# Optimization experiments

Hardware: AMD Instinct MI355X
Metric: run time of the kernel (lower is better)

Reference implementation:

```python
import jax, jax.numpy as jnp
import numpy as np

R, N, F, H, C = 3, 100000, 256, 128, 2
N0, S1, D1, S2, D2 = 16384, 16384, 4096, 4096, 512


def setup_inputs() -> dict:
    key = jax.random.key(0)
    ks = jax.random.split(key, 13)
    return {
        "features": jax.random.normal(ks[0], (N, F), jnp.float32),
        "src_nodes": jax.random.randint(ks[1], (R, N0), 0, N),
        "dstsrc2src1": jax.random.randint(ks[2], (R, S1), 0, N0),
        "dstsrc2dst1": jax.random.randint(ks[3], (R, D1), 0, N0),
        "dif_mat1": jax.random.uniform(ks[4], (R, D1, S1), jnp.float32) / S1,
        "dstsrc2src2": jax.random.randint(ks[5], (R, S2), 0, D1),
        "dstsrc2dst2": jax.random.randint(ks[6], (R, D2), 0, D1),
        "dif_mat2": jax.random.uniform(ks[7], (R, D2, S2), jnp.float32) / S2,
        "w1": jax.random.normal(ks[8], (2 * F, H), jnp.float32) * 0.05,
        "w2": jax.random.normal(ks[9], (2 * H, H), jnp.float32) * 0.05,
        "relation_vectors": jax.random.uniform(ks[10], (R, H), jnp.float32),
        "attention_vec": jax.random.uniform(ks[11], (2 * H, 1), jnp.float32),
        "classifier_w": jax.random.normal(ks[12], (H, C), jnp.float32) * 0.05,
    }


def _agg(x, d2s, d2d, dif, w, rel_vec, att_vec):
    # x: [n, din]; dif: [d, s]; w: [2*din, H]
    agg = dif @ x[d2s]                                  # mean-diffused neighbor feats [d, din]
    h = jnp.concatenate([agg, x[d2d]], axis=1) @ w      # [d, H]
    rel = jnp.broadcast_to(rel_vec[None, :], (h.shape[0], rel_vec.shape[0]))
    score = (jnp.concatenate([h, rel], axis=1) @ att_vec)[:, 0]  # [d]
    att = jax.nn.softmax(score)                         # softmax over batch nodes
    return h * att[:, None]


def reference(features, src_nodes, dstsrc2src1, dstsrc2dst1, dif_mat1,
              dstsrc2src2, dstsrc2dst2, dif_mat2, w1, w2,
              relation_vectors, attention_vec, classifier_w):
    def per_relation(src, s1, d1, m1, s2, d2, m2, rel_vec):
        x = features[src]                               # gather node feats [N0, F]
        x = _agg(x, s1, d1, m1, w1, rel_vec, attention_vec)   # [D1, H]
        x = _agg(x, s2, d2, m2, w2, rel_vec, attention_vec)   # [D2, H]
        return x

    xs = jax.vmap(per_relation)(src_nodes, dstsrc2src1, dstsrc2dst1, dif_mat1,
                                dstsrc2src2, dstsrc2dst2, dif_mat2, relation_vectors)
    summed = jnp.sum(xs, axis=0)                        # sum over relations [D2, H]
    inv_norm = jax.lax.rsqrt(jnp.maximum(jnp.sum(summed * summed, axis=1, keepdims=True), 1e-12))
    normed = summed * inv_norm                          # tf.nn.l2_normalize(axis=1)
    return jax.nn.softmax(normed @ classifier_w, axis=-1)
```

## Files before the change

### kernel.cpp

```cpp
#include <hip/hip_runtime.h>
#include <hip/hip_bf16.h>
#include <math.h>

constexpr int Rc  = 3;
constexpr int Fc  = 256;
constexpr int Hc  = 128;
constexpr int N0c = 16384;
constexpr int S1c = 16384;
constexpr int D1c = 4096;
constexpr int S2c = 4096;
constexpr int D2c = 512;
constexpr int KH1 = 4;
constexpr int KH2 = 16;

typedef __bf16 bf16x8 __attribute__((ext_vector_type(8)));
typedef float  f32x4  __attribute__((ext_vector_type(4)));

__device__ __forceinline__ void glds16(const void* g, void* l) {
  __builtin_amdgcn_global_load_lds(
      (const __attribute__((address_space(1))) void*)g,
      (__attribute__((address_space(3))) void*)l, 16, 0, 0);
}

__device__ __forceinline__ bf16x8 cvt2(const float4 a, const float4 b) {
  bf16x8 c;
  c[0] = (__bf16)a.x; c[1] = (__bf16)a.y; c[2] = (__bf16)a.z; c[3] = (__bf16)a.w;
  c[4] = (__bf16)b.x; c[5] = (__bf16)b.y; c[6] = (__bf16)b.z; c[7] = (__bf16)b.w;
  return c;
}

__device__ __forceinline__ unsigned short bfbits(float v) {
  __bf16 b = (__bf16)v; unsigned short u;
  __builtin_memcpy(&u, &b, 2); return u;
}

__global__ __launch_bounds__(256, 2)
void wpack(const float* __restrict__ w1, const float* __restrict__ w2,
           unsigned char* __restrict__ wp) {
  const int tile = blockIdx.x, half = blockIdx.y, t = threadIdx.x;
  const float* src; int row0;
  if (tile < 4)       { src = w1; row0 = tile * 64; }
  else if (tile < 8)  { src = w1; row0 = 256 + (tile - 4) * 64; }
  else if (tile < 10) { src = w2; row0 = (tile - 8) * 64; }
  else                { src = w2; row0 = 128 + (tile - 10) * 64; }
  unsigned char* dst = wp + ((size_t)half * 12 + tile) * 16384;
  __shared__ float sm[64][132];
  {
    const int r = t >> 2, c0 = (t & 3) * 32;
#pragma unroll
    for (int j = 0; j < 8; j++)
      *(float4*)&sm[r][c0 + 4 * j] = *(const float4*)(src + (size_t)(row0 + r) * 128 + c0 + 4 * j);
  }
  __syncthreads();
  if (t < 128) {
    const int n = t;
#pragma unroll
    for (int ch = 0; ch < 8; ch++) {
      bf16x8 o;
#pragma unroll
      for (int e = 0; e < 8; e++) {
        float v = sm[ch * 8 + e][n];
        __bf16 h = (__bf16)v;
        o[e] = half ? (__bf16)(v - (float)h) : h;
      }
      *(bf16x8*)(dst + n * 128 + ((ch ^ (n & 7)) * 16)) = o;
    }
  }
}

__global__ __launch_bounds__(256, 3)
void gg_layer1(const float* __restrict__ feat, const int* __restrict__ srcn,
               const int* __restrict__ d2s1, const int* __restrict__ d2d1,
               const unsigned char* __restrict__ wp,
               unsigned char* __restrict__ xgwp, float* __restrict__ xdw) {
  const int rel = blockIdx.y;
  int bx = blockIdx.x;
  const int job = bx >= 256 ? 1 : 0;
  if (job) bx -= 256;
  const int s0 = bx * 64;
  const int rows = job ? D1c : S1c;
  const int* idx = job ? d2d1 : d2s1;
  const unsigned char* Bh = wp + (size_t)(job ? 4 : 0) * 16384;
  const unsigned char* Bl = wp + (size_t)(12 + (job ? 4 : 0)) * 16384;

  const int t = threadIdx.x, lane = t & 63, w = t >> 6;
  const int NT = 4;
  const int mh = w >> 1, nh = w & 1;

  __shared__ __bf16 Asm[64 * 64];
  __shared__ __bf16 Bhs[128 * 64];
  __shared__ __bf16 Bls[128 * 64];

  const int arow = t >> 2, ak0 = (t & 3) * 16;
  const int row = s0 + arow;
  const size_t arowg = (size_t)srcn[rel * N0c + idx[(size_t)rel * rows + row]];
  const float* aptr = feat + arowg * Fc + ak0;
  const int ac0 = ak0 >> 3;
  __bf16* asw0 = &Asm[arow * 64 + ((ac0    ) ^ (arow & 7)) * 8];
  __bf16* asw1 = &Asm[arow * 64 + ((ac0 + 1) ^ (arow & 7)) * 8];

  f32x4 acc[2][4] = {};

  for (int tl = 0; tl < NT; ++tl) {
    asm volatile("s_waitcnt lgkmcnt(0)" ::: "memory");
    __builtin_amdgcn_s_barrier();
    __builtin_amdgcn_sched_barrier(0);
    {
      const unsigned char* bh = Bh + (size_t)tl * 16384 + w * 4096 + lane * 16;
      const unsigned char* bl = Bl + (size_t)tl * 16384 + w * 4096 + lane * 16;
      char* dh = (char*)Bhs + w * 4096;
      char* dl = (char*)Bls + w * 4096;
#pragma unroll
      for (int i = 0; i < 4; i++) glds16(bh + i * 1024, dh + i * 1024);
#pragma unroll
      for (int i = 0; i < 4; i++) glds16(bl + i * 1024, dl + i * 1024);
    }
    {
      float4 a[4];
#pragma unroll
      for (int j = 0; j < 4; j++) a[j] = *(const float4*)(aptr + tl * 64 + 4 * j);
      *(bf16x8*)asw0 = cvt2(a[0], a[1]);
      *(bf16x8*)asw1 = cvt2(a[2], a[3]);
    }
    asm volatile("s_waitcnt vmcnt(0) lgkmcnt(0)" ::: "memory");
    __builtin_amdgcn_s_barrier();
    __builtin_amdgcn_sched_barrier(0);
#pragma unroll
    for (int ks = 0; ks < 2; ks++) {
      const int ch = ks * 4 + (lane >> 4);
      bf16x8 af[2], bh[4], bl[4];
#pragma unroll
      for (int mi = 0; mi < 2; mi++) {
        int r = mh * 32 + mi * 16 + (lane & 15);
        af[mi] = *(const bf16x8*)&Asm[r * 64 + ((ch ^ (r & 7)) * 8)];
      }
#pragma unroll
      for (int ni = 0; ni < 4; ni++) {
        int n = nh * 64 + ni * 16 + (lane & 15);
        bh[ni] = *(const bf16x8*)&Bhs[n * 64 + ((ch ^ (n & 7)) * 8)];
        bl[ni] = *(const bf16x8*)&Bls[n * 64 + ((ch ^ (n & 7)) * 8)];
      }
#pragma unroll
      for (int mi = 0; mi < 2; mi++)
#pragma unroll
        for (int ni = 0; ni < 4; ni++) {
          acc[mi][ni] = __builtin_amdgcn_mfma_f32_16x16x32_bf16(af[mi], bh[ni], acc[mi][ni], 0, 0, 0);
          acc[mi][ni] = __builtin_amdgcn_mfma_f32_16x16x32_bf16(af[mi], bl[ni], acc[mi][ni], 0, 0, 0);
        }
    }
  }
  if (job) {
#pragma unroll
    for (int mi = 0; mi < 2; mi++)
#pragma unroll
      for (int ni = 0; ni < 4; ni++) {
        const int col = nh * 64 + ni * 16 + (lane & 15);
#pragma unroll
        for (int j = 0; j < 4; j++) {
          const int r = mh * 32 + mi * 16 + (lane >> 4) * 4 + j;
          xdw[((size_t)rel * D1c + s0 + r) * 128 + col] = acc[mi][ni][j];
        }
      }
  } else {
    unsigned char* tile = xgwp + ((size_t)(rel * (S1c >> 6) + bx)) * 16384;
#pragma unroll
    for (int mi = 0; mi < 2; mi++)
#pragma unroll
      for (int ni = 0; ni < 4; ni++) {
        const int sl0 = mh * 32 + mi * 16 + (lane >> 4) * 4;
        const int n = nh * 64 + ni * 16 + (lane & 15);
        const int ch = sl0 >> 3, e0 = sl0 & 7, cs = ch ^ (n & 7);
        ushort4 u;
        u.x = bfbits(acc[mi][ni][0]); u.y = bfbits(acc[mi][ni][1]);
        u.z = bfbits(acc[mi][ni][2]); u.w = bfbits(acc[mi][ni][3]);
        *(ushort4*)(tile + n * 128 + cs * 16 + e0 * 2) = u;
      }
  }
}

__global__ __launch_bounds__(256, 3)
void gg_layer2(const float* __restrict__ h1, const float* __restrict__ scl,
               const unsigned char* __restrict__ wp,
               float* __restrict__ P, float* __restrict__ Q) {
  const int rel = blockIdx.y, s0 = blockIdx.x * 64, z = blockIdx.z;
  const unsigned char* Bh = wp + (size_t)(z ? 10 : 8) * 16384;
  const unsigned char* Bl = wp + (size_t)(z ? 22 : 20) * 16384;
  float* Cf = z ? Q : P;

  const int t = threadIdx.x, lane = t & 63, w = t >> 6;
  const int NT = 2;
  const int mh = w >> 1, nh = w & 1;

  __shared__ __bf16 Asm[64 * 64];
  __shared__ __bf16 Bhs[128 * 64];
  __shared__ __bf16 Bls[128 * 64];

  const int arow = t >> 2, ak0 = (t & 3) * 16;
  const int row = s0 + arow;
  const float* aptr = h1 + ((size_t)rel * D1c + row) * Hc + ak0;
  const float sc = scl[(size_t)rel * D1c + row];
  const int ac0 = ak0 >> 3;
  __bf16* asw0 = &Asm[arow * 64 + ((ac0    ) ^ (arow & 7)) * 8];
  __bf16* asw1 = &Asm[arow * 64 + ((ac0 + 1) ^ (arow & 7)) * 8];

  f32x4 acc[2][4] = {};

  for (int tl = 0; tl < NT; ++tl) {
    asm volatile("s_waitcnt lgkmcnt(0)" ::: "memory");
    __builtin_amdgcn_s_barrier();
    __builtin_amdgcn_sched_barrier(0);
    {
      const unsigned char* bh = Bh + (size_t)tl * 16384 + w * 4096 + lane * 16;
      const unsigned char* bl = Bl + (size_t)tl * 16384 + w * 4096 + lane * 16;
      char* dh = (char*)Bhs + w * 4096;
      char* dl = (char*)Bls + w * 4096;
#pragma unroll
      for (int i = 0; i < 4; i++) glds16(bh + i * 1024, dh + i * 1024);
#pragma unroll
      for (int i = 0; i < 4; i++) glds16(bl + i * 1024, dl + i * 1024);
    }
    {
      float4 a[4];
#pragma unroll
      for (int j = 0; j < 4; j++) a[j] = *(const float4*)(aptr + tl * 64 + 4 * j);
#pragma unroll
      for (int j = 0; j < 4; j++) { a[j].x *= sc; a[j].y *= sc; a[j].z *= sc; a[j].w *= sc; }
      *(bf16x8*)asw0 = cvt2(a[0], a[1]);
      *(bf16x8*)asw1 = cvt2(a[2], a[3]);
    }
    asm volatile("s_waitcnt vmcnt(0) lgkmcnt(0)" ::: "memory");
    __builtin_amdgcn_s_barrier();
    __builtin_amdgcn_sched_barrier(0);
#pragma unroll
    for (int ks = 0; ks < 2; ks++) {
      const int ch = ks * 4 + (lane >> 4);
      bf16x8 af[2], bh[4], bl[4];
#pragma unroll
      for (int mi = 0; mi < 2; mi++) {
        int r = mh * 32 + mi * 16 + (lane & 15);
        af[mi] = *(const bf16x8*)&Asm[r * 64 + ((ch ^ (r & 7)) * 8)];
      }
#pragma unroll
      for (int ni = 0; ni < 4; ni++) {
        int n = nh * 64 + ni * 16 + (lane & 15);
        bh[ni] = *(const bf16x8*)&Bhs[n * 64 + ((ch ^ (n & 7)) * 8)];
        bl[ni] = *(const bf16x8*)&Bls[n * 64 + ((ch ^ (n & 7)) * 8)];
      }
#pragma unroll
      for (int mi = 0; mi < 2; mi++)
#pragma unroll
        for (int ni = 0; ni < 4; ni++) {
          acc[mi][ni] = __builtin_amdgcn_mfma_f32_16x16x32_bf16(af[mi], bh[ni], acc[mi][ni], 0, 0, 0);
          acc[mi][ni] = __builtin_amdgcn_mfma_f32_16x16x32_bf16(af[mi], bl[ni], acc[mi][ni], 0, 0, 0);
        }
    }
  }
#pragma unroll
  for (int mi = 0; mi < 2; mi++)
#pragma unroll
    for (int ni = 0; ni < 4; ni++) {
      const int col = nh * 64 + ni * 16 + (lane & 15);
#pragma unroll
      for (int j = 0; j < 4; j++) {
        const int r = mh * 32 + mi * 16 + (lane >> 4) * 4 + j;
        Cf[((size_t)rel * D1c + s0 + r) * 128 + col] = acc[mi][ni][j];
      }
    }
}

template <int SWZ>
__global__ __launch_bounds__(256, 3)
void gemm_big(const float* __restrict__ A, const unsigned char* __restrict__ Bp,
              float* __restrict__ C, int M, int KTOT, int KH) {
  int rel, kh, m0;
  if (SWZ) {
    const int F = blockIdx.x;
    const int xcd = F & 7, r = F >> 3;
    const int sub = r >> 5, m = r & 31;
    const int h = xcd + 8 * sub;
    const int g = h >> 1;
    rel = g >> 2; kh = g & 3;
    m0 = ((h & 1) * 32 + m) * 64;
  } else {
    rel = blockIdx.z; kh = blockIdx.y; m0 = blockIdx.x * 64;
  }
  const int t = threadIdx.x, lane = t & 63, w = t >> 6;
  const int KB = KTOT / KH, NT = KB >> 6;
  const int mh = w >> 1, nh = w & 1;

  const float* Ag = A + ((size_t)rel * M + m0) * KTOT + (size_t)kh * KB;
  const unsigned char* Bt = Bp + ((size_t)rel * (KTOT >> 6) + (size_t)kh * NT) * 16384;
  float* Cg = C + (((size_t)kh * Rc + rel) * M + m0) * 128;

  __shared__ __bf16 Asm[64 * 64];
  __shared__ __bf16 Bsm[2][128 * 64];

  f32x4 acc[2][4] = {};
  const int arow = t >> 2, ak0 = (t & 3) * 16;
  const float* aptr = Ag + (size_t)arow * KTOT + ak0;
  const int ac0 = ak0 >> 3;
  __bf16* asw0 = &Asm[arow * 64 + ((ac0    ) ^ (arow & 7)) * 8];
  __bf16* asw1 = &Asm[arow * 64 + ((ac0 + 1) ^ (arow & 7)) * 8];
  const unsigned char* bsrc = Bt + w * 4096 + lane * 16;

  float4 a0[4], a1[4];
#pragma unroll
  for (int j = 0; j < 4; j++) a0[j] = *(const float4*)(aptr + 4 * j);
  {
    char* bd = (char*)Bsm[0] + w * 4096;
#pragma unroll
    for (int i = 0; i < 4; i++) glds16(bsrc + i * 1024, bd + i * 1024);
  }

  for (int tl = 0; tl < NT; ++tl) {
    const int cur = tl & 1;
    asm volatile("s_waitcnt lgkmcnt(0)" ::: "memory");
    __builtin_amdgcn_s_barrier();
    __builtin_amdgcn_sched_barrier(0);
    if (tl + 1 < NT) {
      const unsigned char* bs = bsrc + (size_t)(tl + 1) * 16384;
      char* bd = (char*)Bsm[cur ^ 1] + w * 4096;
#pragma unroll
      for (int i = 0; i < 4; i++) glds16(bs + i * 1024, bd + i * 1024);
      const float* ap = aptr + (size_t)(tl + 1) * 64;
#pragma unroll
      for (int j = 0; j < 4; j++) a1[j] = *(const float4*)(ap + 4 * j);
    }
    *(bf16x8*)asw0 = cvt2(a0[0], a0[1]);
    *(bf16x8*)asw1 = cvt2(a0[2], a0[3]);
    if (tl + 1 < NT)
      asm volatile("s_waitcnt vmcnt(8) lgkmcnt(0)" ::: "memory");
    else
      asm volatile("s_waitcnt vmcnt(0) lgkmcnt(0)" ::: "memory");
    __builtin_amdgcn_s_barrier();
    __builtin_amdgcn_sched_barrier(0);
    const __bf16* Bc = Bsm[cur];
#pragma unroll
    for (int ks = 0; ks < 2; ks++) {
      const int ch = ks * 4 + (lane >> 4);
      bf16x8 af[2], bfr[4];
#pragma unroll
      for (int mi = 0; mi < 2; mi++) {
        int r = mh * 32 + mi * 16 + (lane & 15);
        af[mi] = *(const bf16x8*)&Asm[r * 64 + ((ch ^ (r & 7)) * 8)];
      }
#pragma unroll
      for (int ni = 0; ni < 4; ni++) {
        int n = nh * 64 + ni * 16 + (lane & 15);
        bfr[ni] = *(const bf16x8*)&Bc[n * 64 + ((ch ^ (n & 7)) * 8)];
      }
#pragma unroll
      for (int mi = 0; mi < 2; mi++)
#pragma unroll
        for (int ni = 0; ni < 4; ni++)
          acc[mi][ni] = __builtin_amdgcn_mfma_f32_16x16x32_bf16(af[mi], bfr[ni], acc[mi][ni], 0, 0, 0);
    }
#pragma unroll
    for (int j = 0; j < 4; j++) a0[j] = a1[j];
  }
#pragma unroll
  for (int mi = 0; mi < 2; mi++)
#pragma unroll
    for (int ni = 0; ni < 4; ni++) {
      const int col = nh * 64 + ni * 16 + (lane & 15);
#pragma unroll
      for (int j = 0; j < 4; j++) {
        const int r = mh * 32 + mi * 16 + (lane >> 4) * 4 + j;
        Cg[(size_t)r * 128 + col] = acc[mi][ni][j];
      }
    }
}

__global__ __launch_bounds__(256, 2)
void pgpack(const float* __restrict__ P, const int* __restrict__ d2s2,
            unsigned char* __restrict__ PGp) {
  const int rel = blockIdx.y, kb = blockIdx.x, t = threadIdx.x;
  __shared__ __bf16 sm[64][136];
  {
    const int kl = t >> 2, c0 = (t & 3) * 32;
    const int sr = d2s2[rel * S2c + kb * 64 + kl];
    const float4* p = (const float4*)(P + ((size_t)rel * D1c + sr) * 128 + c0);
#pragma unroll
    for (int j = 0; j < 4; j++)
      *(bf16x8*)&sm[kl][c0 + 8 * j] = cvt2(p[2 * j], p[2 * j + 1]);
  }
  __syncthreads();
  if (t < 128) {
    const int n = t;
    unsigned char* dst = PGp + ((size_t)(rel * (S2c >> 6) + kb)) * 16384;
#pragma unroll
    for (int ch = 0; ch < 8; ch++) {
      bf16x8 o;
#pragma unroll
      for (int e = 0; e < 8; e++) o[e] = sm[ch * 8 + e][n];
      *(bf16x8*)(dst + n * 128 + ((ch ^ (n & 7)) * 16)) = o;
    }
  }
}

__global__ __launch_bounds__(128, 4)
void combine1(const float* __restrict__ aggP, const float* __restrict__ xdw,
              const float* __restrict__ attv, float* __restrict__ h1,
              float* __restrict__ score1) {
  const int rel = blockIdx.y, d0 = blockIdx.x * 8, t = threadIdx.x;
  float acc[8];
#pragma unroll
  for (int i = 0; i < 8; i++) {
    const int d = d0 + i;
    float v = xdw[((size_t)rel * D1c + d) * 128 + t];
#pragma unroll
    for (int p = 0; p < KH1; p++)
      v += aggP[(((size_t)p * Rc + rel) * D1c + d) * 128 + t];
    acc[i] = v;
    h1[((size_t)rel * D1c + d) * 128 + t] = v;
  }
  const float avt = attv[t];
  __shared__ float sred[2][8];
#pragma unroll
  for (int i = 0; i < 8; i++) {
    float p = acc[i] * avt;
    p += __shfl_down(p, 32); p += __shfl_down(p, 16); p += __shfl_down(p, 8);
    p += __shfl_down(p, 4);  p += __shfl_down(p, 2);  p += __shfl_down(p, 1);
    if ((t & 63) == 0) sred[t >> 6][i] = p;
  }
  __syncthreads();
  if (t < 8) score1[rel * D1c + d0 + t] = sred[0][t] + sred[1][t];
}

__global__ __launch_bounds__(128, 4)
void combine2(const float* __restrict__ aggP2, const float* __restrict__ Q,
              const int* __restrict__ d2d2, const float* __restrict__ attv,
              float* __restrict__ h2, float* __restrict__ score2) {
  const int rel = blockIdx.y, d0 = blockIdx.x * 8, t = threadIdx.x;
  float acc[8];
#pragma unroll
  for (int i = 0; i < 8; i++) {
    const int d = d0 + i;
    const int qr = d2d2[rel * D2c + d];
    float v = Q[((size_t)rel * D1c + qr) * 128 + t];
#pragma unroll
    for (int p = 0; p < KH2; p++)
      v += aggP2[(((size_t)p * Rc + rel) * D2c + d) * 128 + t];
    acc[i] = v;
    h2[((size_t)rel * D2c + d) * 128 + t] = v;
  }
  const float avt = attv[t];
  __shared__ float sred[2][8];
#pragma unroll
  for (int i = 0; i < 8; i++) {
    float p = acc[i] * avt;
    p += __shfl_down(p, 32); p += __shfl_down(p, 16); p += __shfl_down(p, 8);
    p += __shfl_down(p, 4);  p += __shfl_down(p, 2);  p += __shfl_down(p, 1);
    if ((t & 63) == 0) sred[t >> 6][i] = p;
  }
  __syncthreads();
  if (t < 8) score2[rel * D2c + d0 + t] = sred[0][t] + sred[1][t];
}

__global__ __launch_bounds__(1024, 1)
void k4_softmax1(float* __restrict__ score1) {
  const int rel = blockIdx.x, t = threadIdx.x;
  float* s = score1 + rel * D1c;
  float v[4], m = -INFINITY;
#pragma unroll
  for (int j = 0; j < 4; j++) { v[j] = s[t + j * 1024]; m = fmaxf(m, v[j]); }
  __shared__ float red[1024];
  red[t] = m; __syncthreads();
  for (int off = 512; off > 0; off >>= 1) {
    if (t < off) red[t] = fmaxf(red[t], red[t + off]);
    __syncthreads();
  }
  const float M = red[0];
  __syncthreads();
  float e[4], sum = 0.f;
#pragma unroll
  for (int j = 0; j < 4; j++) { e[j] = expf(v[j] - M); sum += e[j]; }
  red[t] = sum; __syncthreads();
  for (int off = 512; off > 0; off >>= 1) {
    if (t < off) red[t] += red[t + off];
    __syncthreads();
  }
  const float inv = 1.0f / red[0];
#pragma unroll
  for (int j = 0; j < 4; j++) s[t + j * 1024] = e[j] * inv;
}

__global__ __launch_bounds__(512, 1)
void k8_softmax2(float* __restrict__ score2) {
  const int rel = blockIdx.x, t = threadIdx.x;
  float* s = score2 + rel * D2c;
  const float v = s[t];
  __shared__ float red[512];
  red[t] = v; __syncthreads();
  for (int off = 256; off > 0; off >>= 1) {
    if (t < off) red[t] = fmaxf(red[t], red[t + off]);
    __syncthreads();
  }
  const float M = red[0];
  __syncthreads();
  const float e = expf(v - M);
  red[t] = e; __syncthreads();
  for (int off = 256; off > 0; off >>= 1) {
    if (t < off) red[t] += red[t + off];
    __syncthreads();
  }
  s[t] = e / red[0];
}

__global__ __launch_bounds__(128, 4)
void k9_final(const float* __restrict__ h2, const float* __restrict__ att2,
              const float* __restrict__ cw, float* __restrict__ out) {
  const int d = blockIdx.x, t = threadIdx.x;
  float v = 0.f;
#pragma unroll
  for (int r = 0; r < Rc; r++)
    v += h2[((size_t)r * D2c + d) * Hc + t] * att2[r * D2c + d];
  float ss = v * v;
  ss += __shfl_down(ss, 32); ss += __shfl_down(ss, 16); ss += __shfl_down(ss, 8);
  ss += __shfl_down(ss, 4);  ss += __shfl_down(ss, 2);  ss += __shfl_down(ss, 1);
  __shared__ float sr[3][2];
  if ((t & 63) == 0) sr[0][t >> 6] = ss;
  __syncthreads();
  const float tot = sr[0][0] + sr[0][1];
  const float inv = rsqrtf(fmaxf(tot, 1e-12f));
  const float nv = v * inv;
  float p0 = nv * cw[t * 2], p1 = nv * cw[t * 2 + 1];
  p0 += __shfl_down(p0, 32); p0 += __shfl_down(p0, 16); p0 += __shfl_down(p0, 8);
  p0 += __shfl_down(p0, 4);  p0 += __shfl_down(p0, 2);  p0 += __shfl_down(p0, 1);
  p1 += __shfl_down(p1, 32); p1 += __shfl_down(p1, 16); p1 += __shfl_down(p1, 8);
  p1 += __shfl_down(p1, 4);  p1 += __shfl_down(p1, 2);  p1 += __shfl_down(p1, 1);
  if ((t & 63) == 0) { sr[1][t >> 6] = p0; sr[2][t >> 6] = p1; }
  __syncthreads();
  if (t == 0) {
    const float l0 = sr[1][0] + sr[1][1];
    const float l1 = sr[2][0] + sr[2][1];
    const float m = fmaxf(l0, l1);
    const float e0 = expf(l0 - m), e1 = expf(l1 - m);
    const float is = 1.0f / (e0 + e1);
    out[d * 2 + 0] = e0 * is;
    out[d * 2 + 1] = e1 * is;
  }
}

extern "C" void kernel_launch(void* const* d_in, const int* in_sizes, int n_in,
                              void* d_out, int out_size, void* d_ws, size_t ws_size,
                              hipStream_t stream) {
  (void)in_sizes; (void)n_in; (void)out_size; (void)ws_size;
  const float* feat = (const float*)d_in[0];
  const int*   srcn = (const int*)d_in[1];
  const int*   d2s1 = (const int*)d_in[2];
  const int*   d2d1 = (const int*)d_in[3];
  const float* dif1 = (const float*)d_in[4];
  const int*   d2s2 = (const int*)d_in[5];
  const int*   d2d2 = (const int*)d_in[6];
  const float* dif2 = (const float*)d_in[7];
  const float* w1   = (const float*)d_in[8];
  const float* w2   = (const float*)d_in[9];
  const float* attv = (const float*)d_in[11];
  const float* cw   = (const float*)d_in[12];
  float* out = (float*)d_out;

  char* p = (char*)d_ws;
  auto take = [&](size_t n) { char* r = p; p += (n + 255) & ~(size_t)255; return r; };
  unsigned char* wp   = (unsigned char*)take(24 * 16384);
  unsigned char* xgwp = (unsigned char*)take((size_t)Rc * 256 * 16384);
  float* xdw    = (float*)take((size_t)Rc * D1c * 128 * 4);
  float* aggP   = (float*)take((size_t)KH1 * Rc * D1c * 128 * 4);
  float* h1     = (float*)take((size_t)Rc * D1c * 128 * 4);
  float* score1 = (float*)take((size_t)Rc * D1c * 4);
  unsigned char* PGp = (unsigned char*)take((size_t)Rc * 64 * 16384);
  float* h2     = (float*)take((size_t)Rc * D2c * 128 * 4);
  float* score2 = (float*)take((size_t)Rc * D2c * 4);
  float* P = (float*)xgwp;
  float* Q = P + (size_t)Rc * D1c * 128;
  float* aggP2 = aggP;

  wpack<<<dim3(12, 2), 256, 0, stream>>>(w1, w2, wp);
  gg_layer1<<<dim3(320, Rc), 256, 0, stream>>>(feat, srcn, d2s1, d2d1, wp, xgwp, xdw);
  gemm_big<1><<<768, 256, 0, stream>>>(dif1, xgwp, aggP, D1c, S1c, KH1);
  combine1<<<dim3(D1c / 8, Rc), 128, 0, stream>>>(aggP, xdw, attv, h1, score1);
  k4_softmax1<<<Rc, 1024, 0, stream>>>(score1);
  gg_layer2<<<dim3(D1c / 64, Rc, 2), 256, 0, stream>>>(h1, score1, wp, P, Q);
  pgpack<<<dim3(S2c / 64, Rc), 256, 0, stream>>>(P, d2s2, PGp);
  gemm_big<0><<<dim3(D2c / 64, KH2, Rc), 256, 0, stream>>>(dif2, PGp, aggP2, D2c, S2c, KH2);
  combine2<<<dim3(D2c / 8, Rc), 128, 0, stream>>>(aggP2, Q, d2d2, attv, h2, score2);
  k8_softmax2<<<Rc, 512, 0, stream>>>(score2);
  k9_final<<<D2c, 128, 0, stream>>>(h2, score2, cw, out);
}
```

Baseline: 285.0 us.

## Fuse layer-1 combine into layer-2 GEMM and defer softmax normalization

Merges combine1 and gg_layer2 into one kernel. It sums the K-split partials with xdw, computes the attention score and exp, and runs both layer-2 GEMMs directly from shared memory. The two softmax kernels go away: exp scores are accumulated by atomicAdd into per-relation sums, and the 1/sum scale is applied later in pgpack, combine2 and k9_final, since the scale commutes with the linear layer. This cuts several launches and the h1 write/read round trip, and gg_layer1 now issues all of its A loads up front. The cost is that max subtraction is skipped, so exp could overflow for large scores, and the floating-point atomics make the sums non-deterministic.

```diff
diff --git a/kernel.cpp b/kernel.cpp
--- a/kernel.cpp
+++ b/kernel.cpp
@@ -36,8 +36,9 @@
 
 __global__ __launch_bounds__(256, 2)
 void wpack(const float* __restrict__ w1, const float* __restrict__ w2,
-           unsigned char* __restrict__ wp) {
+           unsigned char* __restrict__ wp, float* __restrict__ esum) {
   const int tile = blockIdx.x, half = blockIdx.y, t = threadIdx.x;
+  if (tile == 0 && half == 0 && t < 8) esum[t] = 0.f;
   const float* src; int row0;
   if (tile < 4)       { src = w1; row0 = tile * 64; }
   else if (tile < 8)  { src = w1; row0 = 256 + (tile - 4) * 64; }
@@ -84,7 +85,6 @@
   const unsigned char* Bl = wp + (size_t)(12 + (job ? 4 : 0)) * 16384;
 
   const int t = threadIdx.x, lane = t & 63, w = t >> 6;
-  const int NT = 4;
   const int mh = w >> 1, nh = w & 1;
 
   __shared__ __bf16 Asm[64 * 64];
@@ -99,9 +99,15 @@
   __bf16* asw0 = &Asm[arow * 64 + ((ac0    ) ^ (arow & 7)) * 8];
   __bf16* asw1 = &Asm[arow * 64 + ((ac0 + 1) ^ (arow & 7)) * 8];
 
+  float4 a[16];
+#pragma unroll
+  for (int tl = 0; tl < 4; tl++)
+#pragma unroll
+    for (int j = 0; j < 4; j++) a[tl * 4 + j] = *(const float4*)(aptr + tl * 64 + 4 * j);
+
   f32x4 acc[2][4] = {};
 
-  for (int tl = 0; tl < NT; ++tl) {
+  for (int tl = 0; tl < 4; ++tl) {
     asm volatile("s_waitcnt lgkmcnt(0)" ::: "memory");
     __builtin_amdgcn_s_barrier();
     __builtin_amdgcn_sched_barrier(0);
@@ -115,13 +121,8 @@
 #pragma unroll
       for (int i = 0; i < 4; i++) glds16(bl + i * 1024, dl + i * 1024);
     }
-    {
-      float4 a[4];
-#pragma unroll
-      for (int j = 0; j < 4; j++) a[j] = *(const float4*)(aptr + tl * 64 + 4 * j);
-      *(bf16x8*)asw0 = cvt2(a[0], a[1]);
-      *(bf16x8*)asw1 = cvt2(a[2], a[3]);
-    }
+    *(bf16x8*)asw0 = cvt2(a[tl * 4 + 0], a[tl * 4 + 1]);
+    *(bf16x8*)asw1 = cvt2(a[tl * 4 + 2], a[tl * 4 + 3]);
     asm volatile("s_waitcnt vmcnt(0) lgkmcnt(0)" ::: "memory");
     __builtin_amdgcn_s_barrier();
     __builtin_amdgcn_sched_barrier(0);
@@ -176,96 +177,6 @@
         *(ushort4*)(tile + n * 128 + cs * 16 + e0 * 2) = u;
       }
   }
-}
-
-__global__ __launch_bounds__(256, 3)
-void gg_layer2(const float* __restrict__ h1, const float* __restrict__ scl,
-               const unsigned char* __restrict__ wp,
-               float* __restrict__ P, float* __restrict__ Q) {
-  const int rel = blockIdx.y, s0 = blockIdx.x * 64, z = blockIdx.z;
-  const unsigned char* Bh = wp + (size_t)(z ? 10 : 8) * 16384;
-  const unsigned char* Bl = wp + (size_t)(z ? 22 : 20) * 16384;
-  float* Cf = z ? Q : P;
-
-  const int t = threadIdx.x, lane = t & 63, w = t >> 6;
-  const int NT = 2;
-  const int mh = w >> 1, nh = w & 1;
-
-  __shared__ __bf16 Asm[64 * 64];
-  __shared__ __bf16 Bhs[128 * 64];
-  __shared__ __bf16 Bls[128 * 64];
-
-  const int arow = t >> 2, ak0 = (t & 3) * 16;
-  const int row = s0 + arow;
-  const float* aptr = h1 + ((size_t)rel * D1c + row) * Hc + ak0;
-  const float sc = scl[(size_t)rel * D1c + row];
-  const int ac0 = ak0 >> 3;
-  __bf16* asw0 = &Asm[arow * 64 + ((ac0    ) ^ (arow & 7)) * 8];
-  __bf16* asw1 = &Asm[arow * 64 + ((ac0 + 1) ^ (arow & 7)) * 8];
-
-  f32x4 acc[2][4] = {};
-
-  for (int tl = 0; tl < NT; ++tl) {
-    asm volatile("s_waitcnt lgkmcnt(0)" ::: "memory");
-    __builtin_amdgcn_s_barrier();
-    __builtin_amdgcn_sched_barrier(0);
-    {
-      const unsigned char* bh = Bh + (size_t)tl * 16384 + w * 4096 + lane * 16;
-      const unsigned char* bl = Bl + (size_t)tl * 16384 + w * 4096 + lane * 16;
-      char* dh = (char*)Bhs + w * 4096;
-      char* dl = (char*)Bls + w * 4096;
-#pragma unroll
-      for (int i = 0; i < 4; i++) glds16(bh + i * 1024, dh + i * 1024);
-#pragma unroll
-      for (int i = 0; i < 4; i++) glds16(bl + i * 1024, dl + i * 1024);
-    }
-    {
-      float4 a[4];
-#pragma unroll
-      for (int j = 0; j < 4; j++) a[j] = *(const float4*)(aptr + tl * 64 + 4 * j);
-#pragma unroll
-      for (int j = 0; j < 4; j++) { a[j].x *= sc; a[j].y *= sc; a[j].z *= sc; a[j].w *= sc; }
-      *(bf16x8*)asw0 = cvt2(a[0], a[1]);
-      *(bf16x8*)asw1 = cvt2(a[2], a[3]);
-    }
-    asm volatile("s_waitcnt vmcnt(0) lgkmcnt(0)" ::: "memory");
-    __builtin_amdgcn_s_barrier();
-    __builtin_amdgcn_sched_barrier(0);
-#pragma unroll
-    for (int ks = 0; ks < 2; ks++) {
-      const int ch = ks * 4 + (lane >> 4);
-      bf16x8 af[2], bh[4], bl[4];
-#pragma unroll
-      for (int mi = 0; mi < 2; mi++) {
-        int r = mh * 32 + mi * 16 + (lane & 15);
-        af[mi] = *(const bf16x8*)&Asm[r * 64 + ((ch ^ (r & 7)) * 8)];
-      }
-#pragma unroll
-      for (int ni = 0; ni < 4; ni++) {
-        int n = nh * 64 + ni * 16 + (lane & 15);
-        bh[ni] = *(const bf16x8*)&Bhs[n * 64 + ((ch ^ (n & 7)) * 8)];
-        bl[ni] = *(const bf16x8*)&Bls[n * 64 + ((ch ^ (n & 7)) * 8)];
-      }
-#pragma unroll
-      for (int mi = 0; mi < 2; mi++)
-#pragma unroll
-        for (int ni = 0; ni < 4; ni++) {
-          acc[mi][ni] = __builtin_amdgcn_mfma_f32_16x16x32_bf16(af[mi], bh[ni], acc[mi][ni], 0, 0, 0);
-          acc[mi][ni] = __builtin_amdgcn_mfma_f32_16x16x32_bf16(af[mi], bl[ni], acc[mi][ni], 0, 0, 0);
-        }
-    }
-  }
-#pragma unroll
-  for (int mi = 0; mi < 2; mi++)
-#pragma unroll
-    for (int ni = 0; ni < 4; ni++) {
-      const int col = nh * 64 + ni * 16 + (lane & 15);
-#pragma unroll
-      for (int j = 0; j < 4; j++) {
-        const int r = mh * 32 + mi * 16 + (lane >> 4) * 4 + j;
-        Cf[((size_t)rel * D1c + s0 + r) * 128 + col] = acc[mi][ni][j];
-      }
-    }
 }
 
 template <int SWZ>
@@ -371,18 +282,140 @@
     }
 }
 
+__global__ __launch_bounds__(256, 3)
+void c1_l2(const float* __restrict__ aggP, const float* __restrict__ xdw,
+           const float* __restrict__ attv, const unsigned char* __restrict__ wp,
+           float* __restrict__ escore1, float* __restrict__ esum,
+           float* __restrict__ P, float* __restrict__ Q) {
+  const int rel = blockIdx.y, d0 = blockIdx.x * 64;
+  const int t = threadIdx.x, lane = t & 63, w = t >> 6;
+  const int mh = w >> 1, nh = w & 1;
+
+  __shared__ __bf16 Asm[64 * 128];
+  __shared__ __bf16 Bhs[128 * 64];
+  __shared__ __bf16 Bls[128 * 64];
+  __shared__ float  sred[64];
+
+  const int r = t >> 2, c0 = (t & 3) * 32;
+  float4 x0[8];
+  {
+    const size_t base = ((size_t)rel * D1c + d0 + r) * 128 + c0;
+#pragma unroll
+    for (int j = 0; j < 8; j++) x0[j] = *(const float4*)(xdw + base + 4 * j);
+#pragma unroll
+    for (int p2 = 0; p2 < KH1; p2++) {
+      const float* ap = aggP + (((size_t)p2 * Rc + rel) * D1c + d0 + r) * 128 + c0;
+#pragma unroll
+      for (int j = 0; j < 8; j++) {
+        float4 u = *(const float4*)(ap + 4 * j);
+        x0[j].x += u.x; x0[j].y += u.y; x0[j].z += u.z; x0[j].w += u.w;
+      }
+    }
+  }
+  float sp = 0.f;
+#pragma unroll
+  for (int j = 0; j < 8; j++) {
+    sp += x0[j].x * attv[c0 + 4 * j]     + x0[j].y * attv[c0 + 4 * j + 1]
+        + x0[j].z * attv[c0 + 4 * j + 2] + x0[j].w * attv[c0 + 4 * j + 3];
+  }
+  sp += __shfl_xor(sp, 1); sp += __shfl_xor(sp, 2);
+  const float e = expf(sp);
+  if ((t & 3) == 0) { escore1[(size_t)rel * D1c + d0 + r] = e; sred[r] = e; }
+  const int ch0 = (t & 3) * 4;
+#pragma unroll
+  for (int q = 0; q < 4; q++) {
+    *(bf16x8*)&Asm[r * 128 + (((ch0 + q) ^ (r & 7)) * 8)] = cvt2(x0[2 * q], x0[2 * q + 1]);
+  }
+  __syncthreads();
+  if (t < 64) {
+    float v = sred[t];
+    v += __shfl_down(v, 32); v += __shfl_down(v, 16); v += __shfl_down(v, 8);
+    v += __shfl_down(v, 4);  v += __shfl_down(v, 2);  v += __shfl_down(v, 1);
+    if (t == 0) atomicAdd(esum + rel, v);
+  }
+  f32x4 accP[2][4] = {}, accQ[2][4] = {};
+#pragma unroll
+  for (int z = 0; z < 2; z++) {
+#pragma unroll
+    for (int tl = 0; tl < 2; tl++) {
+      if (!(z == 0 && tl == 0)) {
+        asm volatile("s_waitcnt lgkmcnt(0)" ::: "memory");
+        __builtin_amdgcn_s_barrier();
+        __builtin_amdgcn_sched_barrier(0);
+      }
+      {
+        const unsigned char* bh = wp + (size_t)(8 + z * 2 + tl) * 16384 + w * 4096 + lane * 16;
+        const unsigned char* bl = wp + (size_t)(20 + z * 2 + tl) * 16384 + w * 4096 + lane * 16;
+        char* dh = (char*)Bhs + w * 4096;
+        char* dl = (char*)Bls + w * 4096;
+#pragma unroll
+        for (int i = 0; i < 4; i++) glds16(bh + i * 1024, dh + i * 1024);
+#pragma unroll
+        for (int i = 0; i < 4; i++) glds16(bl + i * 1024, dl + i * 1024);
+      }
+      asm volatile("s_waitcnt vmcnt(0) lgkmcnt(0)" ::: "memory");
+      __builtin_amdgcn_s_barrier();
+      __builtin_amdgcn_sched_barrier(0);
+      f32x4 (*acc)[4] = z ? accQ : accP;
+#pragma unroll
+      for (int ks = 0; ks < 2; ks++) {
+        const int lch = ks * 4 + (lane >> 4);
+        const int ch  = tl * 8 + lch;
+        bf16x8 af[2], bh[4], bl[4];
+#pragma unroll
+        for (int mi = 0; mi < 2; mi++) {
+          int rr = mh * 32 + mi * 16 + (lane & 15);
+          af[mi] = *(const bf16x8*)&Asm[rr * 128 + ((ch ^ (rr & 7)) * 8)];
+        }
+#pragma unroll
+        for (int ni = 0; ni < 4; ni++) {
+          int n = nh * 64 + ni * 16 + (lane & 15);
+          bh[ni] = *(const bf16x8*)&Bhs[n * 64 + ((lch ^ (n & 7)) * 8)];
+          bl[ni] = *(const bf16x8*)&Bls[n * 64 + ((lch ^ (n & 7)) * 8)];
+        }
+#pragma unroll
+        for (int mi = 0; mi < 2; mi++)
+#pragma unroll
+          for (int ni = 0; ni < 4; ni++) {
+            acc[mi][ni] = __builtin_amdgcn_mfma_f32_16x16x32_bf16(af[mi], bh[ni], acc[mi][ni], 0, 0, 0);
+            acc[mi][ni] = __builtin_amdgcn_mfma_f32_16x16x32_bf16(af[mi], bl[ni], acc[mi][ni], 0, 0, 0);
+          }
+      }
+    }
+  }
+#pragma unroll
+  for (int mi = 0; mi < 2; mi++)
+#pragma unroll
+    for (int ni = 0; ni < 4; ni++) {
+      const int col = nh * 64 + ni * 16 + (lane & 15);
+#pragma unroll
+      for (int j = 0; j < 4; j++) {
+        const int rr = mh * 32 + mi * 16 + (lane >> 4) * 4 + j;
+        P[((size_t)rel * D1c + d0 + rr) * 128 + col] = accP[mi][ni][j];
+        Q[((size_t)rel * D1c + d0 + rr) * 128 + col] = accQ[mi][ni][j];
+      }
+    }
+}
+
 __global__ __launch_bounds__(256, 2)
 void pgpack(const float* __restrict__ P, const int* __restrict__ d2s2,
+            const float* __restrict__ escore1, const float* __restrict__ esum,
             unsigned char* __restrict__ PGp) {
   const int rel = blockIdx.y, kb = blockIdx.x, t = threadIdx.x;
+  const float inv1 = 1.0f / esum[rel];
   __shared__ __bf16 sm[64][136];
   {
     const int kl = t >> 2, c0 = (t & 3) * 32;
     const int sr = d2s2[rel * S2c + kb * 64 + kl];
+    const float sc = escore1[(size_t)rel * D1c + sr] * inv1;
     const float4* p = (const float4*)(P + ((size_t)rel * D1c + sr) * 128 + c0);
 #pragma unroll
-    for (int j = 0; j < 4; j++)
-      *(bf16x8*)&sm[kl][c0 + 8 * j] = cvt2(p[2 * j], p[2 * j + 1]);
+    for (int j = 0; j < 4; j++) {
+      float4 v0 = p[2 * j], v1 = p[2 * j + 1];
+      v0.x *= sc; v0.y *= sc; v0.z *= sc; v0.w *= sc;
+      v1.x *= sc; v1.y *= sc; v1.z *= sc; v1.w *= sc;
+      *(bf16x8*)&sm[kl][c0 + 8 * j] = cvt2(v0, v1);
+    }
   }
   __syncthreads();
   if (t < 128) {
@@ -399,20 +432,24 @@
 }
 
 __global__ __launch_bounds__(128, 4)
-void combine1(const float* __restrict__ aggP, const float* __restrict__ xdw,
-              const float* __restrict__ attv, float* __restrict__ h1,
-              float* __restrict__ score1) {
+void combine2(const float* __restrict__ aggP2, const float* __restrict__ Q,
+              const int* __restrict__ d2d2, const float* __restrict__ attv,
+              const float* __restrict__ escore1, const float* __restrict__ esum,
+              float* __restrict__ h2, float* __restrict__ escore2) {
   const int rel = blockIdx.y, d0 = blockIdx.x * 8, t = threadIdx.x;
+  const float inv1 = 1.0f / esum[rel];
   float acc[8];
 #pragma unroll
   for (int i = 0; i < 8; i++) {
     const int d = d0 + i;
-    float v = xdw[((size_t)rel * D1c + d) * 128 + t];
-#pragma unroll
-    for (int p = 0; p < KH1; p++)
-      v += aggP[(((size_t)p * Rc + rel) * D1c + d) * 128 + t];
+    const int qr = d2d2[rel * D2c + d];
+    const float qs = escore1[(size_t)rel * D1c + qr] * inv1;
+    float v = Q[((size_t)rel * D1c + qr) * 128 + t] * qs;
+#pragma unroll
+    for (int p = 0; p < KH2; p++)
+      v += aggP2[(((size_t)p * Rc + rel) * D2c + d) * 128 + t];
     acc[i] = v;
-    h1[((size_t)rel * D1c + d) * 128 + t] = v;
+    h2[((size_t)rel * D2c + d) * 128 + t] = v;
   }
   const float avt = attv[t];
   __shared__ float sred[2][8];
@@ -424,97 +461,26 @@
     if ((t & 63) == 0) sred[t >> 6][i] = p;
   }
   __syncthreads();
-  if (t < 8) score1[rel * D1c + d0 + t] = sred[0][t] + sred[1][t];
+  if (t < 8) {
+    const float e2 = expf(sred[0][t] + sred[1][t]);
+    escore2[rel * D2c + d0 + t] = e2;
+    float v = e2;
+    v += __shfl_down(v, 4); v += __shfl_down(v, 2); v += __shfl_down(v, 1);
+    if (t == 0) atomicAdd((float*)esum + 4 + rel, v);
+  }
 }
 
 __global__ __launch_bounds__(128, 4)
-void combine2(const float* __restrict__ aggP2, const float* __restrict__ Q,
-              const int* __restrict__ d2d2, const float* __restrict__ attv,
-              float* __restrict__ h2, float* __restrict__ score2) {
-  const int rel = blockIdx.y, d0 = blockIdx.x * 8, t = threadIdx.x;
-  float acc[8];
-#pragma unroll
-  for (int i = 0; i < 8; i++) {
-    const int d = d0 + i;
-    const int qr = d2d2[rel * D2c + d];
-    float v = Q[((size_t)rel * D1c + qr) * 128 + t];
-#pragma unroll
-    for (int p = 0; p < KH2; p++)
-      v += aggP2[(((size_t)p * Rc + rel) * D2c + d) * 128 + t];
-    acc[i] = v;
-    h2[((size_t)rel * D2c + d) * 128 + t] = v;
-  }
-  const float avt = attv[t];
-  __shared__ float sred[2][8];
-#pragma unroll
-  for (int i = 0; i < 8; i++) {
-    float p = acc[i] * avt;
-    p += __shfl_down(p, 32); p += __shfl_down(p, 16); p += __shfl_down(p, 8);
-    p += __shfl_down(p, 4);  p += __shfl_down(p, 2);  p += __shfl_down(p, 1);
-    if ((t & 63) == 0) sred[t >> 6][i] = p;
-  }
-  __syncthreads();
-  if (t < 8) score2[rel * D2c + d0 + t] = sred[0][t] + sred[1][t];
-}
-
-__global__ __launch_bounds__(1024, 1)
-void k4_softmax1(float* __restrict__ score1) {
-  const int rel = blockIdx.x, t = threadIdx.x;
-  float* s = score1 + rel * D1c;
-  float v[4], m = -INFINITY;
-#pragma unroll
-  for (int j = 0; j < 4; j++) { v[j] = s[t + j * 1024]; m = fmaxf(m, v[j]); }
-  __shared__ float red[1024];
-  red[t] = m; __syncthreads();
-  for (int off = 512; off > 0; off >>= 1) {
-    if (t < off) red[t] = fmaxf(red[t], red[t + off]);
-    __syncthreads();
-  }
-  const float M = red[0];
-  __syncthreads();
-  float e[4], sum = 0.f;
-#pragma unroll
-  for (int j = 0; j < 4; j++) { e[j] = expf(v[j] - M); sum += e[j]; }
-  red[t] = sum; __syncthreads();
-  for (int off = 512; off > 0; off >>= 1) {
-    if (t < off) red[t] += red[t + off];
-    __syncthreads();
-  }
-  const float inv = 1.0f / red[0];
-#pragma unroll
-  for (int j = 0; j < 4; j++) s[t + j * 1024] = e[j] * inv;
-}
-
-__global__ __launch_bounds__(512, 1)
-void k8_softmax2(float* __restrict__ score2) {
-  const int rel = blockIdx.x, t = threadIdx.x;
-  float* s = score2 + rel * D2c;
-  const float v = s[t];
-  __shared__ float red[512];
-  red[t] = v; __syncthreads();
-  for (int off = 256; off > 0; off >>= 1) {
-    if (t < off) red[t] = fmaxf(red[t], red[t + off]);
-    __syncthreads();
-  }
-  const float M = red[0];
-  __syncthreads();
-  const float e = expf(v - M);
-  red[t] = e; __syncthreads();
-  for (int off = 256; off > 0; off >>= 1) {
-    if (t < off) red[t] += red[t + off];
-    __syncthreads();
-  }
-  s[t] = e / red[0];
-}
-
-__global__ __launch_bounds__(128, 4)
-void k9_final(const float* __restrict__ h2, const float* __restrict__ att2,
-              const float* __restrict__ cw, float* __restrict__ out) {
+void k9_final(const float* __restrict__ h2, const float* __restrict__ escore2,
+              const float* __restrict__ esum, const float* __restrict__ cw,
+              float* __restrict__ out) {
   const int d = blockIdx.x, t = threadIdx.x;
   float v = 0.f;
 #pragma unroll
-  for (int r = 0; r < Rc; r++)
-    v += h2[((size_t)r * D2c + d) * Hc + t] * att2[r * D2c + d];
+  for (int r = 0; r < Rc; r++) {
+    const float att = escore2[r * D2c + d] / esum[4 + r];
+    v += h2[((size_t)r * D2c + d) * Hc + t] * att;
+  }
   float ss = v * v;
   ss += __shfl_down(ss, 32); ss += __shfl_down(ss, 16); ss += __shfl_down(ss, 8);
   ss += __shfl_down(ss, 4);  ss += __shfl_down(ss, 2);  ss += __shfl_down(ss, 1);
@@ -566,24 +532,21 @@
   unsigned char* xgwp = (unsigned char*)take((size_t)Rc * 256 * 16384);
   float* xdw    = (float*)take((size_t)Rc * D1c * 128 * 4);
   float* aggP   = (float*)take((size_t)KH1 * Rc * D1c * 128 * 4);
-  float* h1     = (float*)take((size_t)Rc * D1c * 128 * 4);
-  float* score1 = (float*)take((size_t)Rc * D1c * 4);
+  float* escore1= (float*)take((size_t)Rc * D1c * 4);
+  float* esum   = (float*)take(256);
   unsigned char* PGp = (unsigned char*)take((size_t)Rc * 64 * 16384);
   float* h2     = (float*)take((size_t)Rc * D2c * 128 * 4);
-  float* score2 = (float*)take((size_t)Rc * D2c * 4);
+  float* escore2= (float*)take((size_t)Rc * D2c * 4);
   float* P = (float*)xgwp;
   float* Q = P + (size_t)Rc * D1c * 128;
   float* aggP2 = aggP;
 
-  wpack<<<dim3(12, 2), 256, 0, stream>>>(w1, w2, wp);
+  wpack<<<dim3(12, 2), 256, 0, stream>>>(w1, w2, wp, esum);
   gg_layer1<<<dim3(320, Rc), 256, 0, stream>>>(feat, srcn, d2s1, d2d1, wp, xgwp, xdw);
   gemm_big<1><<<768, 256, 0, stream>>>(dif1, xgwp, aggP, D1c, S1c, KH1);
-  combine1<<<dim3(D1c / 8, Rc), 128, 0, stream>>>(aggP, xdw, attv, h1, score1);
-  k4_softmax1<<<Rc, 1024, 0, stream>>>(score1);
-  gg_layer2<<<dim3(D1c / 64, Rc, 2), 256, 0, stream>>>(h1, score1, wp, P, Q);
-  pgpack<<<dim3(S2c / 64, Rc), 256, 0, stream>>>(P, d2s2, PGp);
+  c1_l2<<<dim3(D1c / 64, Rc), 256, 0, stream>>>(aggP, xdw, attv, wp, escore1, esum, P, Q);
+  pgpack<<<dim3(S2c / 64, Rc), 256, 0, stream>>>(P, d2s2, escore1, esum, PGp);
   gemm_big<0><<<dim3(D2c / 64, KH2, Rc), 256, 0, stream>>>(dif2, PGp, aggP2, D2c, S2c, KH2);
-  combine2<<<dim3(D2c / 8, Rc), 128, 0, stream>>>(aggP2, Q, d2d2, attv, h2, score2);
-  k8_softmax2<<<Rc, 512, 0, stream>>>(score2);
-  k9_final<<<D2c, 128, 0, stream>>>(h2, score2, cw, out);
-}
+  combine2<<<dim3(D2c / 8, Rc), 128, 0, stream>>>(aggP2, Q, d2d2, attv, escore1, esum, h2, escore2);
+  k9_final<<<D2c, 128, 0, stream>>>(h2, escore2, esum, cw, out);
+}
```

New measurement: 284.9 us. No clear change (-0.0%).
